# Optimization experiments

Hardware: AMD Instinct MI355X
Metric: run time of the kernel (lower is better)

The kernel has to match this reference:

```python
import jax, jax.numpy as jnp
import numpy as np

N_NODES = 50000


def gcn_layer(x, src, dst, W, b):
    # GCNConv: out = D^{-1/2} (A + I) D^{-1/2} (x W) + b
    n = x.shape[0]
    h = x @ W  # [N, C_out]
    # degree including self-loop (count of incoming edges at dst + 1)
    deg = jnp.zeros((n,), dtype=x.dtype).at[dst].add(1.0) + 1.0
    dinv_sqrt = jax.lax.rsqrt(deg)
    norm = dinv_sqrt[src] * dinv_sqrt[dst]  # [E]
    agg = jax.ops.segment_sum(h[src] * norm[:, None], dst, num_segments=n)
    # self-loop contribution: norm_ii = 1/deg_i
    agg = agg + h * (dinv_sqrt * dinv_sqrt)[:, None]
    return agg + b


def setup_inputs() -> dict:
    key = jax.random.key(0)
    k1, k2, k3, k4, k5, k6 = jax.random.split(key, 6)
    in_c, hid_c, out_c = 128, 128, 64
    x = jax.random.normal(k1, (N_NODES, in_c), dtype=jnp.float32)
    edge_index = jax.random.randint(k2, (2, 600000), 0, N_NODES, dtype=jnp.int64)
    W1 = jax.random.normal(k3, (in_c, hid_c), dtype=jnp.float32) * (1.0 / np.sqrt(in_c))
    b1 = jnp.zeros((hid_c,), dtype=jnp.float32)
    W2 = jax.random.normal(k4, (hid_c, out_c), dtype=jnp.float32) * (1.0 / np.sqrt(hid_c))
    b2 = jnp.zeros((out_c,), dtype=jnp.float32)
    return {"x": x, "edge_index": edge_index, "W1": W1, "b1": b1, "W2": W2, "b2": b2}


def reference(x, edge_index, W1, b1, W2, b2):
    src, dst = edge_index[0], edge_index[1]
    h = gcn_layer(x, src, dst, W1, b1)
    h = jax.nn.relu(h)
    out = gcn_layer(h, src, dst, W2, b2)
    return out
```

## Files before the change

kernel.cpp:

```cpp
#include <hip/hip_runtime.h>

#define IN_C 128
#define HID_C 128
#define OUT_C 64
#define CAP 64

typedef unsigned int uint;
typedef unsigned short ushort;
typedef __attribute__((ext_vector_type(8))) short short8;
typedef __attribute__((ext_vector_type(4))) float f32x4;

__device__ __forceinline__ float bf2f(ushort u) {
    return __uint_as_float(((uint)u) << 16);
}
__device__ __forceinline__ ushort f2bf(float f) {
    uint u = __float_as_uint(f);
    return (ushort)((u + 0x7fffu + ((u >> 16) & 1u)) >> 16);
}


__global__ void edge_kernel(const int* __restrict__ src, const int* __restrict__ dst,
                            int* __restrict__ cursor, int* __restrict__ csr_src,
                            int E, int n, int EB,
                            const float* __restrict__ W1, ushort* __restrict__ w1h,
                            ushort* __restrict__ w1l, const float* __restrict__ W2,
                            ushort* __restrict__ w2h, ushort* __restrict__ w2l) {
    int b = blockIdx.x;
    if (b < EB) {
        int e = b * 256 + threadIdx.x;
        if (e < E) {
            unsigned s = (unsigned)src[e];
            unsigned d = (unsigned)dst[e];
            if (s < (unsigned)n && d < (unsigned)n) {
                int p = atomicAdd(&cursor[d], 1);
                if (p < CAP) csr_src[d * CAP + p] = (int)s;
            }
        }
    } else {
        int idx = (b - EB) * 256 + threadIdx.x;
        if (idx < 128 * 128) {
            int k = idx >> 7, c = idx & 127;
            float w = W1[idx];
            ushort h = f2bf(w);
            ushort l = f2bf(w - bf2f(h));
            w1h[c * 128 + k] = h;
            w1l[c * 128 + k] = l;
        } else if (idx < 128 * 128 + 128 * 64) {
            int i2 = idx - 128 * 128;
            int k = i2 >> 6, c = i2 & 63;
            float w = W2[i2];
            ushort h = f2bf(w);
            ushort l = f2bf(w - bf2f(h));
            w2h[c * 128 + k] = h;
            w2l[c * 128 + k] = l;
        }
    }
}


#define LSTR 40

template <int BN>
__global__ __launch_bounds__(256) void gemm_mfma(const float* __restrict__ A,
                                                 const ushort* __restrict__ BTh,
                                                 const ushort* __restrict__ BTl,
                                                 ushort* __restrict__ C, int M) {
    constexpr int K = 128;
    constexpr int NT = BN / 16;
    __shared__ ushort sAh[64 * LSTR], sAl[64 * LSTR];
    __shared__ ushort sBh[BN * LSTR], sBl[BN * LSTR];

    const int tid = threadIdx.x;
    const int w = tid >> 6;
    const int lane = tid & 63;
    const int m = lane & 15;
    const int quad = lane >> 4;
    const int r0 = blockIdx.x * 64;

    f32x4 acc[NT];
#pragma unroll
    for (int t = 0; t < NT; ++t) acc[t] = (f32x4){0.f, 0.f, 0.f, 0.f};

    for (int k0 = 0; k0 < K; k0 += 32) {
#pragma unroll
        for (int it = 0; it < 2; ++it) {
            int idx = tid + it * 256;
            int row = idx >> 3;
            int c4 = idx & 7;
            int grow = r0 + row;
            float4 v = make_float4(0.f, 0.f, 0.f, 0.f);
            if (grow < M) v = *(const float4*)&A[(size_t)grow * K + k0 + c4 * 4];
            ushort h0 = f2bf(v.x), h1 = f2bf(v.y), h2 = f2bf(v.z), h3 = f2bf(v.w);
            ushort l0 = f2bf(v.x - bf2f(h0)), l1 = f2bf(v.y - bf2f(h1));
            ushort l2 = f2bf(v.z - bf2f(h2)), l3 = f2bf(v.w - bf2f(h3));
            *(ushort4*)&sAh[row * LSTR + c4 * 4] = make_ushort4(h0, h1, h2, h3);
            *(ushort4*)&sAl[row * LSTR + c4 * 4] = make_ushort4(l0, l1, l2, l3);
        }
        for (int idx = tid; idx < BN * 4; idx += 256) {
            int row = idx >> 2;
            int c = idx & 3;
            *(uint4*)&sBh[row * LSTR + c * 8] = *(const uint4*)&BTh[row * 128 + k0 + c * 8];
            *(uint4*)&sBl[row * LSTR + c * 8] = *(const uint4*)&BTl[row * 128 + k0 + c * 8];
        }
        __syncthreads();

        short8 ah = *(const short8*)&sAh[(w * 16 + m) * LSTR + quad * 8];
        short8 al = *(const short8*)&sAl[(w * 16 + m) * LSTR + quad * 8];
#pragma unroll
        for (int t = 0; t < NT; ++t) {
            short8 bh = *(const short8*)&sBh[(t * 16 + m) * LSTR + quad * 8];
            short8 bl = *(const short8*)&sBl[(t * 16 + m) * LSTR + quad * 8];
            acc[t] = __builtin_amdgcn_mfma_f32_16x16x32_bf16(ah, bh, acc[t], 0, 0, 0);
            acc[t] = __builtin_amdgcn_mfma_f32_16x16x32_bf16(al, bh, acc[t], 0, 0, 0);
            acc[t] = __builtin_amdgcn_mfma_f32_16x16x32_bf16(ah, bl, acc[t], 0, 0, 0);
        }
        __syncthreads();
    }

#pragma unroll
    for (int t = 0; t < NT; ++t) {
#pragma unroll
        for (int r = 0; r < 4; ++r) {
            int row = r0 + w * 16 + quad * 4 + r;
            if (row < M) C[(size_t)row * BN + t * 16 + m] = f2bf(acc[t][r]);
        }
    }
}


template <int BN>
__global__ __launch_bounds__(256) void gemm_mfma_bf16A(const ushort* __restrict__ A,
                                                       const ushort* __restrict__ BTh,
                                                       const ushort* __restrict__ BTl,
                                                       ushort* __restrict__ C, int M) {
    constexpr int K = 128;
    constexpr int NT = BN / 16;
    __shared__ ushort sA[64 * LSTR];
    __shared__ ushort sBh[BN * LSTR], sBl[BN * LSTR];

    const int tid = threadIdx.x;
    const int w = tid >> 6;
    const int lane = tid & 63;
    const int m = lane & 15;
    const int quad = lane >> 4;
    const int r0 = blockIdx.x * 64;

    f32x4 acc[NT];
#pragma unroll
    for (int t = 0; t < NT; ++t) acc[t] = (f32x4){0.f, 0.f, 0.f, 0.f};

    for (int k0 = 0; k0 < K; k0 += 32) {
        {
            int row = tid >> 2;
            int c = tid & 3;
            int grow = r0 + row;
            uint4 v = make_uint4(0, 0, 0, 0);
            if (grow < M) v = *(const uint4*)&A[(size_t)grow * K + k0 + c * 8];
            *(uint4*)&sA[row * LSTR + c * 8] = v;
        }
        for (int idx = tid; idx < BN * 4; idx += 256) {
            int row = idx >> 2;
            int c = idx & 3;
            *(uint4*)&sBh[row * LSTR + c * 8] = *(const uint4*)&BTh[row * 128 + k0 + c * 8];
            *(uint4*)&sBl[row * LSTR + c * 8] = *(const uint4*)&BTl[row * 128 + k0 + c * 8];
        }
        __syncthreads();

        short8 ah = *(const short8*)&sA[(w * 16 + m) * LSTR + quad * 8];
#pragma unroll
        for (int t = 0; t < NT; ++t) {
            short8 bh = *(const short8*)&sBh[(t * 16 + m) * LSTR + quad * 8];
            short8 bl = *(const short8*)&sBl[(t * 16 + m) * LSTR + quad * 8];
            acc[t] = __builtin_amdgcn_mfma_f32_16x16x32_bf16(ah, bh, acc[t], 0, 0, 0);
            acc[t] = __builtin_amdgcn_mfma_f32_16x16x32_bf16(ah, bl, acc[t], 0, 0, 0);
        }
        __syncthreads();
    }

#pragma unroll
    for (int t = 0; t < NT; ++t) {
#pragma unroll
        for (int r = 0; r < 4; ++r) {
            int row = r0 + w * 16 + quad * 4 + r;
            if (row < M) C[(size_t)row * BN + t * 16 + m] = f2bf(acc[t][r]);
        }
    }
}


__global__ __launch_bounds__(256) void agg128_kernel(
    const ushort4* __restrict__ h4, const int* __restrict__ csr_src,
    const int* __restrict__ degs, const float* __restrict__ bias,
    ushort4* __restrict__ out, int n) {
    int node = blockIdx.x * 4 + (threadIdx.x >> 6);
    if (node >= n) return;
    int lane = threadIdx.x & 63;
    int half = lane >> 5;
    int q = lane & 31;
    int cnt = min(degs[node], CAP);
    float degf = (float)(cnt + 1);
    float dinv_d = rsqrtf(degf);
    int start = node * CAP;
    float a0 = 0.f, a1 = 0.f, a2 = 0.f, a3 = 0.f;

    for (int base = 0; base < cnt; base += 64) {
        int rem = min(cnt - base, 64);
        int es = (lane < rem) ? csr_src[start + base + lane] : 0;
        int cs = (lane < rem) ? degs[es] : 0;
        float en = rsqrtf((float)(cs + 1)) * dinv_d;
        int j = 0;
#define A128_PAIR(J)                                                     \
        {                                                                \
            int s0 = __shfl(es, (J)), s1 = __shfl(es, (J) + 1);          \
            float n0 = __shfl(en, (J)), n1 = __shfl(en, (J) + 1);        \
            int ss = half ? s1 : s0;                                     \
            float nn = half ? n1 : n0;                                   \
            ushort4 v = h4[(size_t)ss * 32 + q];                         \
            a0 += nn * bf2f(v.x); a1 += nn * bf2f(v.y);                  \
            a2 += nn * bf2f(v.z); a3 += nn * bf2f(v.w);                  \
        }
        for (; j + 8 <= rem; j += 8) {
            A128_PAIR(j); A128_PAIR(j + 2); A128_PAIR(j + 4); A128_PAIR(j + 6);
        }
        for (; j + 2 <= rem; j += 2) { A128_PAIR(j); }
        if (j < rem) {
            int s0 = __shfl(es, j);
            float n0 = __shfl(en, j);
            float nn = half ? 0.f : n0;
            ushort4 v = h4[(size_t)s0 * 32 + q];
            a0 += nn * bf2f(v.x); a1 += nn * bf2f(v.y);
            a2 += nn * bf2f(v.z); a3 += nn * bf2f(v.w);
        }
#undef A128_PAIR
    }

    a0 += __shfl_xor(a0, 32);
    a1 += __shfl_xor(a1, 32);
    a2 += __shfl_xor(a2, 32);
    a3 += __shfl_xor(a3, 32);
    if (half == 0) {
        ushort4 sv = h4[(size_t)node * 32 + q];
        float sn = 1.0f / degf;
        float4 bq = ((const float4*)bias)[q];
        a0 = fmaxf(a0 + bf2f(sv.x) * sn + bq.x, 0.f);
        a1 = fmaxf(a1 + bf2f(sv.y) * sn + bq.y, 0.f);
        a2 = fmaxf(a2 + bf2f(sv.z) * sn + bq.z, 0.f);
        a3 = fmaxf(a3 + bf2f(sv.w) * sn + bq.w, 0.f);
        out[(size_t)node * 32 + q] = make_ushort4(f2bf(a0), f2bf(a1), f2bf(a2), f2bf(a3));
    }
}


__global__ __launch_bounds__(256) void agg64_kernel(
    const ushort4* __restrict__ h4, const int* __restrict__ csr_src,
    const int* __restrict__ degs, const float* __restrict__ bias,
    float* __restrict__ out, int n) {
    int node = blockIdx.x * 4 + (threadIdx.x >> 6);
    if (node >= n) return;
    int lane = threadIdx.x & 63;
    int quarter = lane >> 4;
    int q = lane & 15;
    int cnt = min(degs[node], CAP);
    float degf = (float)(cnt + 1);
    float dinv_d = rsqrtf(degf);
    int start = node * CAP;
    float a0 = 0.f, a1 = 0.f, a2 = 0.f, a3 = 0.f;

    for (int base = 0; base < cnt; base += 64) {
        int rem = min(cnt - base, 64);
        int es = (lane < rem) ? csr_src[start + base + lane] : 0;
        int cs = (lane < rem) ? degs[es] : 0;
        float en = rsqrtf((float)(cs + 1)) * dinv_d;
        int j = 0;
#define A64_QUAD(J)                                                          \
        {                                                                    \
            int s0 = __shfl(es, (J)), s1 = __shfl(es, (J) + 1);              \
            int s2 = __shfl(es, (J) + 2), s3 = __shfl(es, (J) + 3);          \
            float n0 = __shfl(en, (J)), n1 = __shfl(en, (J) + 1);            \
            float n2 = __shfl(en, (J) + 2), n3 = __shfl(en, (J) + 3);        \
            int ss = (quarter & 2) ? ((quarter & 1) ? s3 : s2)               \
                                   : ((quarter & 1) ? s1 : s0);              \
            float nn = (quarter & 2) ? ((quarter & 1) ? n3 : n2)             \
                                     : ((quarter & 1) ? n1 : n0);            \
            ushort4 v = h4[(size_t)ss * 16 + q];                             \
            a0 += nn * bf2f(v.x); a1 += nn * bf2f(v.y);                      \
            a2 += nn * bf2f(v.z); a3 += nn * bf2f(v.w);                      \
        }
        for (; j + 8 <= rem; j += 8) { A64_QUAD(j); A64_QUAD(j + 4); }
        if (j + 4 <= rem) { A64_QUAD(j); j += 4; }
#undef A64_QUAD
        if (j < rem) {
            int k = j + quarter;
            int valid = (k < rem);
            int kk = valid ? k : j;
            int ss = __shfl(es, kk);
            float nv = __shfl(en, kk);
            float nn = valid ? nv : 0.f;
            ushort4 v = h4[(size_t)ss * 16 + q];
            a0 += nn * bf2f(v.x); a1 += nn * bf2f(v.y);
            a2 += nn * bf2f(v.z); a3 += nn * bf2f(v.w);
        }
    }

    a0 += __shfl_xor(a0, 16);
    a1 += __shfl_xor(a1, 16);
    a2 += __shfl_xor(a2, 16);
    a3 += __shfl_xor(a3, 16);
    a0 += __shfl_xor(a0, 32);
    a1 += __shfl_xor(a1, 32);
    a2 += __shfl_xor(a2, 32);
    a3 += __shfl_xor(a3, 32);
    if (quarter == 0) {
        ushort4 sv = h4[(size_t)node * 16 + q];
        float sn = 1.0f / degf;
        float4 bq = ((const float4*)bias)[q];
        float4 o;
        o.x = a0 + bf2f(sv.x) * sn + bq.x;
        o.y = a1 + bf2f(sv.y) * sn + bq.y;
        o.z = a2 + bf2f(sv.z) * sn + bq.z;
        o.w = a3 + bf2f(sv.w) * sn + bq.w;
        ((float4*)out)[(size_t)node * 16 + q] = o;
    }
}


extern "C" void kernel_launch(void* const* d_in, const int* in_sizes, int n_in,
                              void* d_out, int out_size, void* d_ws, size_t ws_size,
                              hipStream_t stream) {
    (void)n_in; (void)out_size; (void)ws_size;
    const float* x  = (const float*)d_in[0];
    const int*   ei = (const int*)d_in[1];
    const float* W1 = (const float*)d_in[2];
    const float* b1 = (const float*)d_in[3];
    const float* W2 = (const float*)d_in[4];
    const float* b2 = (const float*)d_in[5];
    float* out = (float*)d_out;

    const int n = in_sizes[0] / IN_C;
    const int E = in_sizes[1] / 2;
    const int* src = ei;
    const int* dst = ei + E;

    char* ws = (char*)d_ws;
    size_t off = 0;
    auto alloc = [&](size_t bytes) -> void* {
        void* p = ws + off;
        off += (bytes + 1023) & ~(size_t)1023;
        return p;
    };

    ushort* w1h     = (ushort*)alloc(128 * 128 * 2);
    ushort* w1l     = (ushort*)alloc(128 * 128 * 2);
    ushort* w2h     = (ushort*)alloc(64 * 128 * 2);
    ushort* w2l     = (ushort*)alloc(64 * 128 * 2);
    size_t  npad    = ((size_t)n * 4 + 1023) & ~(size_t)1023;
    int*    cursor  = (int*)   alloc(npad);
    int*    csr_src = (int*)   alloc((size_t)n * CAP * 4);
    ushort* h1      = (ushort*)alloc((size_t)n * HID_C * 2);
    ushort* h2      = h1;
    ushort* out1b   = (ushort*)alloc((size_t)n * HID_C * 2);

    hipMemsetAsync(cursor, 0, npad, stream);

    const int EB = (E + 255) / 256;
    const int SB = (128 * 128 + 128 * 64 + 255) / 256;
    edge_kernel<<<EB + SB, 256, 0, stream>>>(src, dst, cursor, csr_src, E, n, EB,
                                             W1, w1h, w1l, W2, w2h, w2l);

    const int gblocks = (n + 63) / 64;
    const int ablocks = (n + 3) / 4;
    gemm_mfma<HID_C><<<gblocks, 256, 0, stream>>>(x, w1h, w1l, h1, n);
    agg128_kernel<<<ablocks, 256, 0, stream>>>((const ushort4*)h1, csr_src, cursor,
                                               b1, (ushort4*)out1b, n);
    gemm_mfma_bf16A<OUT_C><<<gblocks, 256, 0, stream>>>(out1b, w2h, w2l, h2, n);
    agg64_kernel<<<ablocks, 256, 0, stream>>>((const ushort4*)h2, csr_src, cursor,
                                              b2, out, n);
}
```

Before: 186.8 us.

## Fuse all GCN stages into one persistent cooperative kernel with grid syncs

Replaces the memset plus five separate kernel launches with a single cooperative kernel. Inside it, the phases (cursor zeroing, CSR build and weight split, GEMM1, aggregation 1, GEMM2, aggregation 2) are separated by grid-wide syncs and run as grid-stride loops over a grid sized from occupancy and capped at 1024 blocks. The aim is to remove launch gaps and memset overhead between stages. In exchange it adds grid barrier costs, possible lower occupancy from the larger shared-memory footprint, and fewer blocks than the original per-stage grids, which may hurt latency hiding in the gather-heavy aggregation phases.

```diff
diff --git a/kernel.cpp b/kernel.cpp
--- a/kernel.cpp
+++ b/kernel.cpp
@@ -1,4 +1,7 @@
 #include <hip/hip_runtime.h>
+#include <hip/hip_cooperative_groups.h>
+
+namespace cg = cooperative_groups;
 
 #define IN_C 128
 #define HID_C 128
@@ -18,308 +21,293 @@
     return (ushort)((u + 0x7fffu + ((u >> 16) & 1u)) >> 16);
 }
 
-
-__global__ void edge_kernel(const int* __restrict__ src, const int* __restrict__ dst,
-                            int* __restrict__ cursor, int* __restrict__ csr_src,
-                            int E, int n, int EB,
-                            const float* __restrict__ W1, ushort* __restrict__ w1h,
-                            ushort* __restrict__ w1l, const float* __restrict__ W2,
-                            ushort* __restrict__ w2h, ushort* __restrict__ w2l) {
-    int b = blockIdx.x;
-    if (b < EB) {
-        int e = b * 256 + threadIdx.x;
-        if (e < E) {
-            unsigned s = (unsigned)src[e];
-            unsigned d = (unsigned)dst[e];
-            if (s < (unsigned)n && d < (unsigned)n) {
-                int p = atomicAdd(&cursor[d], 1);
-                if (p < CAP) csr_src[d * CAP + p] = (int)s;
-            }
-        }
-    } else {
-        int idx = (b - EB) * 256 + threadIdx.x;
+__global__ __launch_bounds__(256) void fused_kernel(
+    const float* __restrict__ x, const int* __restrict__ src, const int* __restrict__ dst,
+    const float* __restrict__ W1, const float* __restrict__ b1,
+    const float* __restrict__ W2, const float* __restrict__ b2,
+    int* __restrict__ cursor, int* __restrict__ csr_src,
+    ushort* __restrict__ w1h, ushort* __restrict__ w1l,
+    ushort* __restrict__ w2h, ushort* __restrict__ w2l,
+    ushort* __restrict__ h, ushort* __restrict__ out1b, float* __restrict__ out,
+    int n, int E) {
+    cg::grid_group grid = cg::this_grid();
+    __shared__ ushort smem[15360];
+
+    const int tid = threadIdx.x;
+    const int gsz = gridDim.x * 256;
+    const int gtid = blockIdx.x * 256 + tid;
+
+    for (int i = gtid; i < n; i += gsz) cursor[i] = 0;
+    grid.sync();
+
+    for (int e = gtid; e < E; e += gsz) {
+        unsigned s = (unsigned)src[e];
+        unsigned d = (unsigned)dst[e];
+        if (s < (unsigned)n && d < (unsigned)n) {
+            int p = atomicAdd(&cursor[d], 1);
+            if (p < CAP) csr_src[d * CAP + p] = (int)s;
+        }
+    }
+    for (int idx = gtid; idx < 128 * 128 + 128 * 64; idx += gsz) {
         if (idx < 128 * 128) {
             int k = idx >> 7, c = idx & 127;
             float w = W1[idx];
-            ushort h = f2bf(w);
-            ushort l = f2bf(w - bf2f(h));
-            w1h[c * 128 + k] = h;
-            w1l[c * 128 + k] = l;
-        } else if (idx < 128 * 128 + 128 * 64) {
+            ushort hh = f2bf(w);
+            ushort ll = f2bf(w - bf2f(hh));
+            w1h[c * 128 + k] = hh;
+            w1l[c * 128 + k] = ll;
+        } else {
             int i2 = idx - 128 * 128;
             int k = i2 >> 6, c = i2 & 63;
             float w = W2[i2];
-            ushort h = f2bf(w);
-            ushort l = f2bf(w - bf2f(h));
-            w2h[c * 128 + k] = h;
-            w2l[c * 128 + k] = l;
-        }
-    }
-}
-
-
-#define LSTR 40
-
-template <int BN>
-__global__ __launch_bounds__(256) void gemm_mfma(const float* __restrict__ A,
-                                                 const ushort* __restrict__ BTh,
-                                                 const ushort* __restrict__ BTl,
-                                                 ushort* __restrict__ C, int M) {
-    constexpr int K = 128;
-    constexpr int NT = BN / 16;
-    __shared__ ushort sAh[64 * LSTR], sAl[64 * LSTR];
-    __shared__ ushort sBh[BN * LSTR], sBl[BN * LSTR];
-
-    const int tid = threadIdx.x;
+            ushort hh = f2bf(w);
+            ushort ll = f2bf(w - bf2f(hh));
+            w2h[c * 128 + k] = hh;
+            w2l[c * 128 + k] = ll;
+        }
+    }
+    grid.sync();
+
     const int w = tid >> 6;
     const int lane = tid & 63;
     const int m = lane & 15;
     const int quad = lane >> 4;
-    const int r0 = blockIdx.x * 64;
-
-    f32x4 acc[NT];
-#pragma unroll
-    for (int t = 0; t < NT; ++t) acc[t] = (f32x4){0.f, 0.f, 0.f, 0.f};
-
-    for (int k0 = 0; k0 < K; k0 += 32) {
-#pragma unroll
-        for (int it = 0; it < 2; ++it) {
-            int idx = tid + it * 256;
-            int row = idx >> 3;
-            int c4 = idx & 7;
-            int grow = r0 + row;
-            float4 v = make_float4(0.f, 0.f, 0.f, 0.f);
-            if (grow < M) v = *(const float4*)&A[(size_t)grow * K + k0 + c4 * 4];
-            ushort h0 = f2bf(v.x), h1 = f2bf(v.y), h2 = f2bf(v.z), h3 = f2bf(v.w);
-            ushort l0 = f2bf(v.x - bf2f(h0)), l1 = f2bf(v.y - bf2f(h1));
-            ushort l2 = f2bf(v.z - bf2f(h2)), l3 = f2bf(v.w - bf2f(h3));
-            *(ushort4*)&sAh[row * LSTR + c4 * 4] = make_ushort4(h0, h1, h2, h3);
-            *(ushort4*)&sAl[row * LSTR + c4 * 4] = make_ushort4(l0, l1, l2, l3);
-        }
-        for (int idx = tid; idx < BN * 4; idx += 256) {
-            int row = idx >> 2;
-            int c = idx & 3;
-            *(uint4*)&sBh[row * LSTR + c * 8] = *(const uint4*)&BTh[row * 128 + k0 + c * 8];
-            *(uint4*)&sBl[row * LSTR + c * 8] = *(const uint4*)&BTl[row * 128 + k0 + c * 8];
-        }
-        __syncthreads();
-
-        short8 ah = *(const short8*)&sAh[(w * 16 + m) * LSTR + quad * 8];
-        short8 al = *(const short8*)&sAl[(w * 16 + m) * LSTR + quad * 8];
-#pragma unroll
-        for (int t = 0; t < NT; ++t) {
-            short8 bh = *(const short8*)&sBh[(t * 16 + m) * LSTR + quad * 8];
-            short8 bl = *(const short8*)&sBl[(t * 16 + m) * LSTR + quad * 8];
-            acc[t] = __builtin_amdgcn_mfma_f32_16x16x32_bf16(ah, bh, acc[t], 0, 0, 0);
-            acc[t] = __builtin_amdgcn_mfma_f32_16x16x32_bf16(al, bh, acc[t], 0, 0, 0);
-            acc[t] = __builtin_amdgcn_mfma_f32_16x16x32_bf16(ah, bl, acc[t], 0, 0, 0);
-        }
-        __syncthreads();
-    }
-
-#pragma unroll
-    for (int t = 0; t < NT; ++t) {
-#pragma unroll
-        for (int r = 0; r < 4; ++r) {
-            int row = r0 + w * 16 + quad * 4 + r;
-            if (row < M) C[(size_t)row * BN + t * 16 + m] = f2bf(acc[t][r]);
-        }
-    }
-}
-
-
-template <int BN>
-__global__ __launch_bounds__(256) void gemm_mfma_bf16A(const ushort* __restrict__ A,
-                                                       const ushort* __restrict__ BTh,
-                                                       const ushort* __restrict__ BTl,
-                                                       ushort* __restrict__ C, int M) {
-    constexpr int K = 128;
-    constexpr int NT = BN / 16;
-    __shared__ ushort sA[64 * LSTR];
-    __shared__ ushort sBh[BN * LSTR], sBl[BN * LSTR];
-
-    const int tid = threadIdx.x;
-    const int w = tid >> 6;
-    const int lane = tid & 63;
-    const int m = lane & 15;
-    const int quad = lane >> 4;
-    const int r0 = blockIdx.x * 64;
-
-    f32x4 acc[NT];
-#pragma unroll
-    for (int t = 0; t < NT; ++t) acc[t] = (f32x4){0.f, 0.f, 0.f, 0.f};
-
-    for (int k0 = 0; k0 < K; k0 += 32) {
-        {
-            int row = tid >> 2;
-            int c = tid & 3;
-            int grow = r0 + row;
-            uint4 v = make_uint4(0, 0, 0, 0);
-            if (grow < M) v = *(const uint4*)&A[(size_t)grow * K + k0 + c * 8];
-            *(uint4*)&sA[row * LSTR + c * 8] = v;
-        }
-        for (int idx = tid; idx < BN * 4; idx += 256) {
-            int row = idx >> 2;
-            int c = idx & 3;
-            *(uint4*)&sBh[row * LSTR + c * 8] = *(const uint4*)&BTh[row * 128 + k0 + c * 8];
-            *(uint4*)&sBl[row * LSTR + c * 8] = *(const uint4*)&BTl[row * 128 + k0 + c * 8];
-        }
-        __syncthreads();
-
-        short8 ah = *(const short8*)&sA[(w * 16 + m) * LSTR + quad * 8];
-#pragma unroll
-        for (int t = 0; t < NT; ++t) {
-            short8 bh = *(const short8*)&sBh[(t * 16 + m) * LSTR + quad * 8];
-            short8 bl = *(const short8*)&sBl[(t * 16 + m) * LSTR + quad * 8];
-            acc[t] = __builtin_amdgcn_mfma_f32_16x16x32_bf16(ah, bh, acc[t], 0, 0, 0);
-            acc[t] = __builtin_amdgcn_mfma_f32_16x16x32_bf16(ah, bl, acc[t], 0, 0, 0);
-        }
-        __syncthreads();
-    }
-
-#pragma unroll
-    for (int t = 0; t < NT; ++t) {
-#pragma unroll
-        for (int r = 0; r < 4; ++r) {
-            int row = r0 + w * 16 + quad * 4 + r;
-            if (row < M) C[(size_t)row * BN + t * 16 + m] = f2bf(acc[t][r]);
-        }
-    }
-}
-
-
-__global__ __launch_bounds__(256) void agg128_kernel(
-    const ushort4* __restrict__ h4, const int* __restrict__ csr_src,
-    const int* __restrict__ degs, const float* __restrict__ bias,
-    ushort4* __restrict__ out, int n) {
-    int node = blockIdx.x * 4 + (threadIdx.x >> 6);
-    if (node >= n) return;
-    int lane = threadIdx.x & 63;
-    int half = lane >> 5;
-    int q = lane & 31;
-    int cnt = min(degs[node], CAP);
-    float degf = (float)(cnt + 1);
-    float dinv_d = rsqrtf(degf);
-    int start = node * CAP;
-    float a0 = 0.f, a1 = 0.f, a2 = 0.f, a3 = 0.f;
-
-    for (int base = 0; base < cnt; base += 64) {
-        int rem = min(cnt - base, 64);
-        int es = (lane < rem) ? csr_src[start + base + lane] : 0;
-        int cs = (lane < rem) ? degs[es] : 0;
-        float en = rsqrtf((float)(cs + 1)) * dinv_d;
-        int j = 0;
+    const int gblocks = (n + 63) / 64;
+    const int ablocks = (n + 3) / 4;
+
+    {
+        ushort* sAh = smem;
+        ushort* sAl = smem + 2560;
+        ushort* sBh = smem + 5120;
+        ushort* sBl = smem + 10240;
+        for (int tile = blockIdx.x; tile < gblocks; tile += gridDim.x) {
+            const int r0 = tile * 64;
+            f32x4 acc[8];
+#pragma unroll
+            for (int t = 0; t < 8; ++t) acc[t] = (f32x4){0.f, 0.f, 0.f, 0.f};
+            for (int k0 = 0; k0 < 128; k0 += 32) {
+#pragma unroll
+                for (int it = 0; it < 2; ++it) {
+                    int idx = tid + it * 256;
+                    int row = idx >> 3;
+                    int c4 = idx & 7;
+                    int grow = r0 + row;
+                    float4 v = make_float4(0.f, 0.f, 0.f, 0.f);
+                    if (grow < n) v = *(const float4*)&x[(size_t)grow * 128 + k0 + c4 * 4];
+                    ushort h0 = f2bf(v.x), h1 = f2bf(v.y), h2 = f2bf(v.z), h3 = f2bf(v.w);
+                    ushort l0 = f2bf(v.x - bf2f(h0)), l1 = f2bf(v.y - bf2f(h1));
+                    ushort l2 = f2bf(v.z - bf2f(h2)), l3 = f2bf(v.w - bf2f(h3));
+                    *(ushort4*)&sAh[row * 40 + c4 * 4] = make_ushort4(h0, h1, h2, h3);
+                    *(ushort4*)&sAl[row * 40 + c4 * 4] = make_ushort4(l0, l1, l2, l3);
+                }
+                for (int idx = tid; idx < 128 * 4; idx += 256) {
+                    int row = idx >> 2;
+                    int c = idx & 3;
+                    *(uint4*)&sBh[row * 40 + c * 8] = *(const uint4*)&w1h[row * 128 + k0 + c * 8];
+                    *(uint4*)&sBl[row * 40 + c * 8] = *(const uint4*)&w1l[row * 128 + k0 + c * 8];
+                }
+                __syncthreads();
+                short8 ah = *(const short8*)&sAh[(w * 16 + m) * 40 + quad * 8];
+                short8 al = *(const short8*)&sAl[(w * 16 + m) * 40 + quad * 8];
+#pragma unroll
+                for (int t = 0; t < 8; ++t) {
+                    short8 bh = *(const short8*)&sBh[(t * 16 + m) * 40 + quad * 8];
+                    short8 bl = *(const short8*)&sBl[(t * 16 + m) * 40 + quad * 8];
+                    acc[t] = __builtin_amdgcn_mfma_f32_16x16x32_bf16(ah, bh, acc[t], 0, 0, 0);
+                    acc[t] = __builtin_amdgcn_mfma_f32_16x16x32_bf16(al, bh, acc[t], 0, 0, 0);
+                    acc[t] = __builtin_amdgcn_mfma_f32_16x16x32_bf16(ah, bl, acc[t], 0, 0, 0);
+                }
+                __syncthreads();
+            }
+#pragma unroll
+            for (int t = 0; t < 8; ++t) {
+#pragma unroll
+                for (int r = 0; r < 4; ++r) {
+                    int row = r0 + w * 16 + quad * 4 + r;
+                    if (row < n) h[(size_t)row * 128 + t * 16 + m] = f2bf(acc[t][r]);
+                }
+            }
+        }
+    }
+    grid.sync();
+
+    {
+        const ushort4* h4 = (const ushort4*)h;
+        ushort4* o4 = (ushort4*)out1b;
+        int half = lane >> 5;
+        int q = lane & 31;
+        for (int grp = blockIdx.x; grp < ablocks; grp += gridDim.x) {
+            int node = grp * 4 + w;
+            if (node < n) {
+                int cnt = min(cursor[node], CAP);
+                float degf = (float)(cnt + 1);
+                float dinv_d = rsqrtf(degf);
+                int start = node * CAP;
+                float a0 = 0.f, a1 = 0.f, a2 = 0.f, a3 = 0.f;
+                for (int base = 0; base < cnt; base += 64) {
+                    int rem = min(cnt - base, 64);
+                    int es = (lane < rem) ? csr_src[start + base + lane] : 0;
+                    int cs = (lane < rem) ? cursor[es] : 0;
+                    float en = rsqrtf((float)(cs + 1)) * dinv_d;
+                    int j = 0;
 #define A128_PAIR(J)                                                     \
-        {                                                                \
-            int s0 = __shfl(es, (J)), s1 = __shfl(es, (J) + 1);          \
-            float n0 = __shfl(en, (J)), n1 = __shfl(en, (J) + 1);        \
-            int ss = half ? s1 : s0;                                     \
-            float nn = half ? n1 : n0;                                   \
-            ushort4 v = h4[(size_t)ss * 32 + q];                         \
-            a0 += nn * bf2f(v.x); a1 += nn * bf2f(v.y);                  \
-            a2 += nn * bf2f(v.z); a3 += nn * bf2f(v.w);                  \
-        }
-        for (; j + 8 <= rem; j += 8) {
-            A128_PAIR(j); A128_PAIR(j + 2); A128_PAIR(j + 4); A128_PAIR(j + 6);
-        }
-        for (; j + 2 <= rem; j += 2) { A128_PAIR(j); }
-        if (j < rem) {
-            int s0 = __shfl(es, j);
-            float n0 = __shfl(en, j);
-            float nn = half ? 0.f : n0;
-            ushort4 v = h4[(size_t)s0 * 32 + q];
-            a0 += nn * bf2f(v.x); a1 += nn * bf2f(v.y);
-            a2 += nn * bf2f(v.z); a3 += nn * bf2f(v.w);
-        }
+                    {                                                    \
+                        int s0 = __shfl(es, (J)), s1 = __shfl(es, (J) + 1); \
+                        float n0 = __shfl(en, (J)), n1 = __shfl(en, (J) + 1); \
+                        int ss = half ? s1 : s0;                         \
+                        float nn = half ? n1 : n0;                       \
+                        ushort4 v = h4[(size_t)ss * 32 + q];             \
+                        a0 += nn * bf2f(v.x); a1 += nn * bf2f(v.y);      \
+                        a2 += nn * bf2f(v.z); a3 += nn * bf2f(v.w);      \
+                    }
+                    for (; j + 8 <= rem; j += 8) {
+                        A128_PAIR(j); A128_PAIR(j + 2); A128_PAIR(j + 4); A128_PAIR(j + 6);
+                    }
+                    for (; j + 2 <= rem; j += 2) { A128_PAIR(j); }
+                    if (j < rem) {
+                        int s0 = __shfl(es, j);
+                        float n0 = __shfl(en, j);
+                        float nn = half ? 0.f : n0;
+                        ushort4 v = h4[(size_t)s0 * 32 + q];
+                        a0 += nn * bf2f(v.x); a1 += nn * bf2f(v.y);
+                        a2 += nn * bf2f(v.z); a3 += nn * bf2f(v.w);
+                    }
 #undef A128_PAIR
-    }
-
-    a0 += __shfl_xor(a0, 32);
-    a1 += __shfl_xor(a1, 32);
-    a2 += __shfl_xor(a2, 32);
-    a3 += __shfl_xor(a3, 32);
-    if (half == 0) {
-        ushort4 sv = h4[(size_t)node * 32 + q];
-        float sn = 1.0f / degf;
-        float4 bq = ((const float4*)bias)[q];
-        a0 = fmaxf(a0 + bf2f(sv.x) * sn + bq.x, 0.f);
-        a1 = fmaxf(a1 + bf2f(sv.y) * sn + bq.y, 0.f);
-        a2 = fmaxf(a2 + bf2f(sv.z) * sn + bq.z, 0.f);
-        a3 = fmaxf(a3 + bf2f(sv.w) * sn + bq.w, 0.f);
-        out[(size_t)node * 32 + q] = make_ushort4(f2bf(a0), f2bf(a1), f2bf(a2), f2bf(a3));
-    }
-}
-
-
-__global__ __launch_bounds__(256) void agg64_kernel(
-    const ushort4* __restrict__ h4, const int* __restrict__ csr_src,
-    const int* __restrict__ degs, const float* __restrict__ bias,
-    float* __restrict__ out, int n) {
-    int node = blockIdx.x * 4 + (threadIdx.x >> 6);
-    if (node >= n) return;
-    int lane = threadIdx.x & 63;
-    int quarter = lane >> 4;
-    int q = lane & 15;
-    int cnt = min(degs[node], CAP);
-    float degf = (float)(cnt + 1);
-    float dinv_d = rsqrtf(degf);
-    int start = node * CAP;
-    float a0 = 0.f, a1 = 0.f, a2 = 0.f, a3 = 0.f;
-
-    for (int base = 0; base < cnt; base += 64) {
-        int rem = min(cnt - base, 64);
-        int es = (lane < rem) ? csr_src[start + base + lane] : 0;
-        int cs = (lane < rem) ? degs[es] : 0;
-        float en = rsqrtf((float)(cs + 1)) * dinv_d;
-        int j = 0;
+                }
+                a0 += __shfl_xor(a0, 32);
+                a1 += __shfl_xor(a1, 32);
+                a2 += __shfl_xor(a2, 32);
+                a3 += __shfl_xor(a3, 32);
+                if (half == 0) {
+                    ushort4 sv = h4[(size_t)node * 32 + q];
+                    float sn = 1.0f / degf;
+                    float4 bq = ((const float4*)b1)[q];
+                    a0 = fmaxf(a0 + bf2f(sv.x) * sn + bq.x, 0.f);
+                    a1 = fmaxf(a1 + bf2f(sv.y) * sn + bq.y, 0.f);
+                    a2 = fmaxf(a2 + bf2f(sv.z) * sn + bq.z, 0.f);
+                    a3 = fmaxf(a3 + bf2f(sv.w) * sn + bq.w, 0.f);
+                    o4[(size_t)node * 32 + q] = make_ushort4(f2bf(a0), f2bf(a1), f2bf(a2), f2bf(a3));
+                }
+            }
+        }
+    }
+    grid.sync();
+
+    {
+        ushort* sA = smem;
+        ushort* sBh = smem + 2560;
+        ushort* sBl = smem + 5120;
+        for (int tile = blockIdx.x; tile < gblocks; tile += gridDim.x) {
+            const int r0 = tile * 64;
+            f32x4 acc[4];
+#pragma unroll
+            for (int t = 0; t < 4; ++t) acc[t] = (f32x4){0.f, 0.f, 0.f, 0.f};
+            for (int k0 = 0; k0 < 128; k0 += 32) {
+                {
+                    int row = tid >> 2;
+                    int c = tid & 3;
+                    int grow = r0 + row;
+                    uint4 v = make_uint4(0, 0, 0, 0);
+                    if (grow < n) v = *(const uint4*)&out1b[(size_t)grow * 128 + k0 + c * 8];
+                    *(uint4*)&sA[row * 40 + c * 8] = v;
+                }
+                for (int idx = tid; idx < 64 * 4; idx += 256) {
+                    int row = idx >> 2;
+                    int c = idx & 3;
+                    *(uint4*)&sBh[row * 40 + c * 8] = *(const uint4*)&w2h[row * 128 + k0 + c * 8];
+                    *(uint4*)&sBl[row * 40 + c * 8] = *(const uint4*)&w2l[row * 128 + k0 + c * 8];
+                }
+                __syncthreads();
+                short8 ah = *(const short8*)&sA[(w * 16 + m) * 40 + quad * 8];
+#pragma unroll
+                for (int t = 0; t < 4; ++t) {
+                    short8 bh = *(const short8*)&sBh[(t * 16 + m) * 40 + quad * 8];
+                    short8 bl = *(const short8*)&sBl[(t * 16 + m) * 40 + quad * 8];
+                    acc[t] = __builtin_amdgcn_mfma_f32_16x16x32_bf16(ah, bh, acc[t], 0, 0, 0);
+                    acc[t] = __builtin_amdgcn_mfma_f32_16x16x32_bf16(ah, bl, acc[t], 0, 0, 0);
+                }
+                __syncthreads();
+            }
+#pragma unroll
+            for (int t = 0; t < 4; ++t) {
+#pragma unroll
+                for (int r = 0; r < 4; ++r) {
+                    int row = r0 + w * 16 + quad * 4 + r;
+                    if (row < n) h[(size_t)row * 64 + t * 16 + m] = f2bf(acc[t][r]);
+                }
+            }
+        }
+    }
+    grid.sync();
+
+    {
+        const ushort4* h4 = (const ushort4*)h;
+        int quarter = lane >> 4;
+        int q = lane & 15;
+        for (int grp = blockIdx.x; grp < ablocks; grp += gridDim.x) {
+            int node = grp * 4 + w;
+            if (node < n) {
+                int cnt = min(cursor[node], CAP);
+                float degf = (float)(cnt + 1);
+                float dinv_d = rsqrtf(degf);
+                int start = node * CAP;
+                float a0 = 0.f, a1 = 0.f, a2 = 0.f, a3 = 0.f;
+                for (int base = 0; base < cnt; base += 64) {
+                    int rem = min(cnt - base, 64);
+                    int es = (lane < rem) ? csr_src[start + base + lane] : 0;
+                    int cs = (lane < rem) ? cursor[es] : 0;
+                    float en = rsqrtf((float)(cs + 1)) * dinv_d;
+                    int j = 0;
 #define A64_QUAD(J)                                                          \
-        {                                                                    \
-            int s0 = __shfl(es, (J)), s1 = __shfl(es, (J) + 1);              \
-            int s2 = __shfl(es, (J) + 2), s3 = __shfl(es, (J) + 3);          \
-            float n0 = __shfl(en, (J)), n1 = __shfl(en, (J) + 1);            \
-            float n2 = __shfl(en, (J) + 2), n3 = __shfl(en, (J) + 3);        \
-            int ss = (quarter & 2) ? ((quarter & 1) ? s3 : s2)               \
-                                   : ((quarter & 1) ? s1 : s0);              \
-            float nn = (quarter & 2) ? ((quarter & 1) ? n3 : n2)             \
-                                     : ((quarter & 1) ? n1 : n0);            \
-            ushort4 v = h4[(size_t)ss * 16 + q];                             \
-            a0 += nn * bf2f(v.x); a1 += nn * bf2f(v.y);                      \
-            a2 += nn * bf2f(v.z); a3 += nn * bf2f(v.w);                      \
-        }
-        for (; j + 8 <= rem; j += 8) { A64_QUAD(j); A64_QUAD(j + 4); }
-        if (j + 4 <= rem) { A64_QUAD(j); j += 4; }
+                    {                                                        \
+                        int s0 = __shfl(es, (J)), s1 = __shfl(es, (J) + 1);  \
+                        int s2 = __shfl(es, (J) + 2), s3 = __shfl(es, (J) + 3); \
+                        float n0 = __shfl(en, (J)), n1 = __shfl(en, (J) + 1); \
+                        float n2 = __shfl(en, (J) + 2), n3 = __shfl(en, (J) + 3); \
+                        int ss = (quarter & 2) ? ((quarter & 1) ? s3 : s2)   \
+                                               : ((quarter & 1) ? s1 : s0);  \
+                        float nn = (quarter & 2) ? ((quarter & 1) ? n3 : n2) \
+                                                 : ((quarter & 1) ? n1 : n0); \
+                        ushort4 v = h4[(size_t)ss * 16 + q];                 \
+                        a0 += nn * bf2f(v.x); a1 += nn * bf2f(v.y);          \
+                        a2 += nn * bf2f(v.z); a3 += nn * bf2f(v.w);          \
+                    }
+                    for (; j + 8 <= rem; j += 8) { A64_QUAD(j); A64_QUAD(j + 4); }
+                    if (j + 4 <= rem) { A64_QUAD(j); j += 4; }
 #undef A64_QUAD
-        if (j < rem) {
-            int k = j + quarter;
-            int valid = (k < rem);
-            int kk = valid ? k : j;
-            int ss = __shfl(es, kk);
-            float nv = __shfl(en, kk);
-            float nn = valid ? nv : 0.f;
-            ushort4 v = h4[(size_t)ss * 16 + q];
-            a0 += nn * bf2f(v.x); a1 += nn * bf2f(v.y);
-            a2 += nn * bf2f(v.z); a3 += nn * bf2f(v.w);
-        }
-    }
-
-    a0 += __shfl_xor(a0, 16);
-    a1 += __shfl_xor(a1, 16);
-    a2 += __shfl_xor(a2, 16);
-    a3 += __shfl_xor(a3, 16);
-    a0 += __shfl_xor(a0, 32);
-    a1 += __shfl_xor(a1, 32);
-    a2 += __shfl_xor(a2, 32);
-    a3 += __shfl_xor(a3, 32);
-    if (quarter == 0) {
-        ushort4 sv = h4[(size_t)node * 16 + q];
-        float sn = 1.0f / degf;
-        float4 bq = ((const float4*)bias)[q];
-        float4 o;
-        o.x = a0 + bf2f(sv.x) * sn + bq.x;
-        o.y = a1 + bf2f(sv.y) * sn + bq.y;
-        o.z = a2 + bf2f(sv.z) * sn + bq.z;
-        o.w = a3 + bf2f(sv.w) * sn + bq.w;
-        ((float4*)out)[(size_t)node * 16 + q] = o;
+                    if (j < rem) {
+                        int k = j + quarter;
+                        int valid = (k < rem);
+                        int kk = valid ? k : j;
+                        int ss = __shfl(es, kk);
+                        float nv = __shfl(en, kk);
+                        float nn = valid ? nv : 0.f;
+                        ushort4 v = h4[(size_t)ss * 16 + q];
+                        a0 += nn * bf2f(v.x); a1 += nn * bf2f(v.y);
+                        a2 += nn * bf2f(v.z); a3 += nn * bf2f(v.w);
+                    }
+                }
+                a0 += __shfl_xor(a0, 16);
+                a1 += __shfl_xor(a1, 16);
+                a2 += __shfl_xor(a2, 16);
+                a3 += __shfl_xor(a3, 16);
+                a0 += __shfl_xor(a0, 32);
+                a1 += __shfl_xor(a1, 32);
+                a2 += __shfl_xor(a2, 32);
+                a3 += __shfl_xor(a3, 32);
+                if (quarter == 0) {
+                    ushort4 sv = h4[(size_t)node * 16 + q];
+                    float sn = 1.0f / degf;
+                    float4 bq = ((const float4*)b2)[q];
+                    float4 o;
+                    o.x = a0 + bf2f(sv.x) * sn + bq.x;
+                    o.y = a1 + bf2f(sv.y) * sn + bq.y;
+                    o.z = a2 + bf2f(sv.z) * sn + bq.z;
+                    o.w = a3 + bf2f(sv.w) * sn + bq.w;
+                    ((float4*)out)[(size_t)node * 16 + q] = o;
+                }
+            }
+        }
     }
 }
 
@@ -336,8 +324,8 @@
     const float* b2 = (const float*)d_in[5];
     float* out = (float*)d_out;
 
-    const int n = in_sizes[0] / IN_C;
-    const int E = in_sizes[1] / 2;
+    int n = in_sizes[0] / IN_C;
+    int E = in_sizes[1] / 2;
     const int* src = ei;
     const int* dst = ei + E;
 
@@ -353,26 +341,21 @@
     ushort* w1l     = (ushort*)alloc(128 * 128 * 2);
     ushort* w2h     = (ushort*)alloc(64 * 128 * 2);
     ushort* w2l     = (ushort*)alloc(64 * 128 * 2);
-    size_t  npad    = ((size_t)n * 4 + 1023) & ~(size_t)1023;
-    int*    cursor  = (int*)   alloc(npad);
+    int*    cursor  = (int*)   alloc((size_t)n * 4);
     int*    csr_src = (int*)   alloc((size_t)n * CAP * 4);
-    ushort* h1      = (ushort*)alloc((size_t)n * HID_C * 2);
-    ushort* h2      = h1;
+    ushort* h       = (ushort*)alloc((size_t)n * HID_C * 2);
     ushort* out1b   = (ushort*)alloc((size_t)n * HID_C * 2);
 
-    hipMemsetAsync(cursor, 0, npad, stream);
-
-    const int EB = (E + 255) / 256;
-    const int SB = (128 * 128 + 128 * 64 + 255) / 256;
-    edge_kernel<<<EB + SB, 256, 0, stream>>>(src, dst, cursor, csr_src, E, n, EB,
-                                             W1, w1h, w1l, W2, w2h, w2l);
-
-    const int gblocks = (n + 63) / 64;
-    const int ablocks = (n + 3) / 4;
-    gemm_mfma<HID_C><<<gblocks, 256, 0, stream>>>(x, w1h, w1l, h1, n);
-    agg128_kernel<<<ablocks, 256, 0, stream>>>((const ushort4*)h1, csr_src, cursor,
-                                               b1, (ushort4*)out1b, n);
-    gemm_mfma_bf16A<OUT_C><<<gblocks, 256, 0, stream>>>(out1b, w2h, w2l, h2, n);
-    agg64_kernel<<<ablocks, 256, 0, stream>>>((const ushort4*)h2, csr_src, cursor,
-                                              b2, out, n);
+    int maxB = 0;
+    hipOccupancyMaxActiveBlocksPerMultiprocessor(&maxB, fused_kernel, 256, 0);
+    int numCU = 0;
+    hipDeviceGetAttribute(&numCU, hipDeviceAttributeMultiprocessorCount, 0);
+    if (maxB < 1) maxB = 1;
+    if (numCU < 1) numCU = 256;
+    int grid = maxB * numCU;
+    if (grid > 1024) grid = 1024;
+
+    void* args[] = {&x, &src, &dst, &W1, &b1, &W2, &b2, &cursor, &csr_src,
+                    &w1h, &w1l, &w2h, &w2l, &h, &out1b, &out, &n, &E};
+    hipLaunchCooperativeKernel((void*)fused_kernel, dim3(grid), dim3(256), args, 0, stream);
 }
```

Measured after the change: 560.3 us. +200.0%, slower.
